# Optimization experiments

Hardware: AMD Instinct MI355X
Metric: run time of the kernel (lower is better)

The kernel has to match this reference:

```python
import jax, jax.numpy as jnp
import numpy as np

DIM, HEADS = 768, 12
HEAD_DIM = DIM // HEADS
SCALE = HEAD_DIM ** -0.5


def setup_inputs() -> dict:
    key = jax.random.key(0)
    ks = jax.random.split(key, 16)
    B, LQ, LK = 8, 512, 512
    s = DIM ** -0.5
    inp = {
        "query": jax.random.normal(ks[0], (B, LQ, DIM), jnp.float32),
        "key_value": jax.random.normal(ks[1], (B, LK, DIM), jnp.float32),
        "query_coords": jax.random.normal(ks[2], (LQ, 2), jnp.float32),
        "key_coords": jax.random.normal(ks[3], (LK, 2), jnp.float32),
        "Wq": jax.random.normal(ks[4], (DIM, DIM), jnp.float32) * s,
        "bq": jnp.zeros((DIM,), jnp.float32),
        "Wk": jax.random.normal(ks[5], (DIM, DIM), jnp.float32) * s,
        "bk": jnp.zeros((DIM,), jnp.float32),
        "Wv": jax.random.normal(ks[6], (DIM, DIM), jnp.float32) * s,
        "bv": jnp.zeros((DIM,), jnp.float32),
        "Wo": jax.random.normal(ks[7], (DIM, DIM), jnp.float32) * s,
        "bo": jnp.zeros((DIM,), jnp.float32),
        "W1": jax.random.normal(ks[8], (6, DIM), jnp.float32) * (6 ** -0.5),
        "b1": jnp.zeros((DIM,), jnp.float32),
        "W2": jax.random.normal(ks[9], (DIM, HEADS), jnp.float32) * s,
        "b2": jnp.zeros((HEADS,), jnp.float32),
    }
    return inp


def reference(query, key_value, query_coords, key_coords,
              Wq, bq, Wk, bk, Wv, bv, Wo, bo, W1, b1, W2, b2):
    B, LQ, _ = query.shape
    LK = key_value.shape[1]
    # QKV projections -> [B, L, H, Dh]
    q = (query @ Wq + bq).reshape(B, LQ, HEADS, HEAD_DIM)
    k = (key_value @ Wk + bk).reshape(B, LK, HEADS, HEAD_DIM)
    v = (key_value @ Wv + bv).reshape(B, LK, HEADS, HEAD_DIM)
    # attention logits [B, H, LQ, LK]
    logits = jnp.einsum('bqhd,bkhd->bhqk', q, k) * SCALE
    # pairwise relative bias: delta [LQ, LK, 2] -> rel [LQ, LK, 6]
    delta = query_coords[:, None, :] - key_coords[None, :, :]
    rel = jnp.concatenate([delta, jnp.abs(delta), jnp.square(delta)], axis=-1)
    hidden = jax.nn.gelu(rel @ W1 + b1, approximate=False)  # [LQ, LK, DIM]
    bias = hidden @ W2 + b2  # [LQ, LK, H]
    logits = logits + jnp.transpose(bias, (2, 0, 1))[None]  # [B,H,LQ,LK]
    weights = jax.nn.softmax(logits, axis=-1)
    out = jnp.einsum('bhqk,bkhd->bqhd', weights, v).reshape(B, LQ, DIM)
    return out @ Wo + bo
```

## Files before the change

kernel.cpp:

```cpp
#include <hip/hip_runtime.h>
#include <hip/hip_bf16.h>
#include <stdint.h>
#include <math.h>

typedef __attribute__((ext_vector_type(4))) float f32x4;
typedef _Float16 f16;
typedef __attribute__((ext_vector_type(8))) _Float16 f16x8;
typedef decltype(__builtin_amdgcn_cvt_pkrtz(0.f, 0.f)) pk16;

#define DIM   768
#define NH    12
#define HD    64
#define NB    8
#define SEQ   512
#define SCALE 0.125f

#define GN    161
#define GPTS  (GN * GN)

#define MFMA16H __builtin_amdgcn_mfma_f32_16x16x32_f16

struct PrepArgs {
    const float* query; const float* key_value; f16* Xq; f16* Xkv;
    const float* W[4]; f16* WT[4];
    const float* W1; const float* b1; const float* W2;
    f16* W1tab; f16* W2tab; float* gtab32;
};

__global__ void __launch_bounds__(256) k_prep(PrepArgs pa) {
    __shared__ float tt[32][33];
    int g = blockIdx.x, t = threadIdx.x;
    if (g < 3072) {
        const float* in = (g < 1536) ? pa.query : pa.key_value;
        f16* out = (g < 1536) ? pa.Xq : pa.Xkv;
        int i = (g % 1536) * 256 + t;
        const float4* s = reinterpret_cast<const float4*>(in + i * 8);
        float4 f0 = s[0], f1 = s[1];
        union { pk16 h[4]; uint4 v; } o;
        o.h[0] = __builtin_amdgcn_cvt_pkrtz(f0.x, f0.y);
        o.h[1] = __builtin_amdgcn_cvt_pkrtz(f0.z, f0.w);
        o.h[2] = __builtin_amdgcn_cvt_pkrtz(f1.x, f1.y);
        o.h[3] = __builtin_amdgcn_cvt_pkrtz(f1.z, f1.w);
        reinterpret_cast<uint4*>(out)[i] = o.v;
    } else if (g < 5376) {
        int bi = g - 3072;
        int z = bi / 576, rem = bi % 576;
        int bx = rem % 24, by = rem / 24;
        const float* W = pa.W[z];
        f16* WT = pa.WT[z];
        int n0 = bx * 32, k0 = by * 32;
        int tx = t & 31, ty = t >> 5;
#pragma unroll
        for (int j = 0; j < 4; ++j)
            tt[ty + 8 * j][tx] = W[(k0 + ty + 8 * j) * DIM + n0 + tx];
        __syncthreads();
#pragma unroll
        for (int j = 0; j < 4; ++j)
            WT[(n0 + ty + 8 * j) * DIM + k0 + tx] = (f16)tt[tx][ty + 8 * j];
    } else {
        int i = (g - 5376) * 256 + t;
        if (i < 3072) {
            int lane = i & 63;
            int hi = lane >> 4, m = lane & 15;
            int u = (i >> 6) * 16 + m;
#pragma unroll
            for (int e = 0; e < 8; ++e) {
                float v = 0.f;
                if (hi == 0) {
                    if (e < 6) v = pa.W1[e * DIM + u];
                    else if (e == 6) v = pa.b1[u];
                }
                pa.W1tab[i * 8 + e] = (f16)v;
            }
        } else if (i < 4608) {
            int i2 = i - 3072;
            int j = i2 >> 6, lane = i2 & 63;
            int gq = lane >> 4, h = lane & 15;
#pragma unroll
            for (int e = 0; e < 8; ++e) {
                int u = 32 * j + ((e >> 2) << 4) + (gq << 2) + (e & 3);
                float v = (h < 12) ? pa.W2[u * 12 + h] : 0.f;
                pa.W2tab[i2 * 8 + e] = (f16)v;
            }
        } else {
            int i2 = i - 4608;
            float x = (i2 + 0.5f) * (1.0f / 256.0f) - 8.0f;
            pa.gtab32[i2] = 0.5f * x * (1.0f + erff(x * 0.70710678f));
        }
    }
}

__global__ void __launch_bounds__(256) k_grid(const f16x8* __restrict__ W1tab,
                                              const f16x8* __restrict__ W2tab,
                                              const float* __restrict__ b2,
                                              const float* __restrict__ gtab32,
                                              f16* __restrict__ grid16) {
    __shared__ float tab[4096];
    int t = threadIdx.x, lane = t & 63, w = t >> 6;
    {
        const uint4* gt = (const uint4*)gtab32;
        uint4* st = (uint4*)tab;
#pragma unroll
        for (int i = 0; i < 4; ++i) st[i * 256 + t] = gt[i * 256 + t];
    }
    int hi = lane >> 4, m = lane & 15;
    int p0 = blockIdx.x * 64 + w * 16;
    int p = p0 + m;
    int gy = p / GN, gx = p - gy * GN;
    float dx = gx * 0.125f - 10.0f;
    float dy = gy * 0.125f - 10.0f;

    union { f16x8 v; pk16 h2[4]; } rf;
    { f16x8 zz = {}; rf.v = zz; }
    if (hi == 0) {
        rf.h2[0] = __builtin_amdgcn_cvt_pkrtz(dx, dy);
        rf.h2[1] = __builtin_amdgcn_cvt_pkrtz(fabsf(dx), fabsf(dy));
        rf.h2[2] = __builtin_amdgcn_cvt_pkrtz(dx * dx, dy * dy);
        rf.h2[3] = __builtin_amdgcn_cvt_pkrtz(1.0f, 0.0f);
    }

    float b2h = (m < 12) ? b2[m] : 0.f;
    f32x4 acc = {b2h, b2h, b2h, b2h};
    const f32x4 zero = {};
    const f16x8* w1p = W1tab + lane;
    const f16x8* w2p = W2tab + lane;
    __syncthreads();

#pragma unroll 2
    for (int j = 0; j < 24; ++j) {
        f16x8 a0  = w1p[(2 * j) * 64];
        f16x8 a1  = w1p[(2 * j + 1) * 64];
        f16x8 w2v = w2p[j * 64];
        f32x4 pre0 = MFMA16H(a0, rf.v, zero, 0, 0, 0);
        f32x4 pre1 = MFMA16H(a1, rf.v, zero, 0, 0, 0);
        float s0[4], s1[4];
#pragma unroll
        for (int e = 0; e < 4; ++e) {
            float x0 = pre0[e];
            float xi0 = __builtin_amdgcn_fmed3f(__builtin_fmaf(x0, 256.f, 2048.f), 0.f, 4095.f);
            float g0 = tab[(int)xi0];
            s0[e] = (x0 > 8.f) ? x0 : g0;
            float x1 = pre1[e];
            float xi1 = __builtin_amdgcn_fmed3f(__builtin_fmaf(x1, 256.f, 2048.f), 0.f, 4095.f);
            float g1 = tab[(int)xi1];
            s1[e] = (x1 > 8.f) ? x1 : g1;
        }
        union { f16x8 v; pk16 h2[4]; } pav;
        pav.h2[0] = __builtin_amdgcn_cvt_pkrtz(s0[0], s0[1]);
        pav.h2[1] = __builtin_amdgcn_cvt_pkrtz(s0[2], s0[3]);
        pav.h2[2] = __builtin_amdgcn_cvt_pkrtz(s1[0], s1[1]);
        pav.h2[3] = __builtin_amdgcn_cvt_pkrtz(s1[2], s1[3]);
        acc = MFMA16H(pav.v, w2v, acc, 0, 0, 0);
    }
    if (m < 12) {
#pragma unroll
        for (int r = 0; r < 4; ++r) {
            int pr = p0 + hi * 4 + r;
            if (pr < GPTS) grid16[pr * 16 + m] = (f16)acc[r];
        }
    }
}

struct MQArgs {
    const float* qc; const float* kc;
    const f16* grid16; f16* bias16;
    const f16* Xq; const f16* Xkv;
    const f16* WqT; const f16* WkT; const f16* WvT;
    const float* bq; const float* bk; const float* bv;
    f16* q_ws; f16* k_ws; f16* v_t;
};

__global__ void __launch_bounds__(256) k_mq3(MQArgs a) {
    __shared__ uint4 lds[1024];
    int bid = blockIdx.x, t = threadIdx.x;
    int lane = t & 63, w = t >> 6;
    int hi = lane >> 4, lm = lane & 15;
    int xcd = bid & 7, slot = bid >> 3;

    if (slot >= 16) {
        int lid = xcd * 288 + (slot - 16);
        int m_group = lid / 36;
        int within = lid - m_group * 36;
        int z = within / 12;
        int n_tile = within - z * 12;
        int m0 = m_group * 64, n0 = n_tile * 64;
        const f16* X = (z == 0) ? a.Xq : a.Xkv;
        const f16* Wt = (z == 0) ? a.WqT : (z == 1) ? a.WkT : a.WvT;
        const float* bias = (z == 0) ? a.bq : (z == 1) ? a.bk : a.bv;
        f16* out = (z == 0) ? a.q_ws : (z == 1) ? a.k_ws : a.v_t;

        int wr = w >> 1, wc = w & 1;
        int srow = t >> 2, sslot = t & 3;
        const f16* Ag = X + (m0 + srow) * DIM + sslot * 8;
        const f16* Bg = Wt + (n0 + srow) * DIM + sslot * 8;
        int wi = srow * 4 + (sslot ^ ((srow >> 1) & 3));

        int aidx[2], bidx[2];
#pragma unroll
        for (int i = 0; i < 2; ++i) {
            int ar = wr * 32 + i * 16 + lm;
            aidx[i] = ar * 4 + (hi ^ ((ar >> 1) & 3));
            int br = wc * 32 + i * 16 + lm;
            bidx[i] = 256 + br * 4 + (hi ^ ((br >> 1) & 3));
        }

        f32x4 acc[2][2] = {};
        lds[wi] = *(const uint4*)(Ag);
        lds[256 + wi] = *(const uint4*)(Bg);
        __syncthreads();

        for (int kt = 0; kt < 24; ++kt) {
            uint4 na, nb;
            bool pf = kt < 23;
            if (pf) {
                na = *(const uint4*)(Ag + (kt + 1) * 32);
                nb = *(const uint4*)(Bg + (kt + 1) * 32);
            }
            int bo = (kt & 1) << 9;
            f16x8 af[2], bf[2];
#pragma unroll
            for (int i = 0; i < 2; ++i) {
                af[i] = *(const f16x8*)&lds[bo + aidx[i]];
                bf[i] = *(const f16x8*)&lds[bo + bidx[i]];
            }
#pragma unroll
            for (int mi = 0; mi < 2; ++mi)
#pragma unroll
                for (int ni = 0; ni < 2; ++ni)
                    acc[mi][ni] = MFMA16H(af[mi], bf[ni], acc[mi][ni], 0, 0, 0);
            if (pf) {
                int bo2 = bo ^ 512;
                lds[bo2 + wi] = na;
                lds[bo2 + 256 + wi] = nb;
                __syncthreads();
            }
        }

#pragma unroll
        for (int mi = 0; mi < 2; ++mi)
#pragma unroll
            for (int ni = 0; ni < 2; ++ni) {
                int n = n0 + wc * 32 + ni * 16 + lm;
                float bn = bias[n];
                int h = n >> 6, d = n & 63;
                int mbase = m0 + wr * 32 + mi * 16 + hi * 4;
                int bb = mbase >> 9, l0 = mbase & 511;
                if (z == 2) {
                    union { pk16 h2[2]; uint2 u2; } o;
                    o.h2[0] = __builtin_amdgcn_cvt_pkrtz(acc[mi][ni][0] + bn, acc[mi][ni][1] + bn);
                    o.h2[1] = __builtin_amdgcn_cvt_pkrtz(acc[mi][ni][2] + bn, acc[mi][ni][3] + bn);
                    *reinterpret_cast<uint2*>(out + (((bb * NH + h) * HD) + d) * SEQ + l0) = o.u2;
                } else {
#pragma unroll
                    for (int r = 0; r < 4; ++r)
                        out[(((bb * NH + h) * SEQ) + l0 + r) * HD + d] = (f16)(acc[mi][ni][r] + bn);
                }
            }
    } else {
        int id = xcd * 16 + slot;
#pragma unroll 2
        for (int i = 0; i < 8; ++i) {
            int p = id * 2048 + i * 256 + t;
            int qi = p >> 9, ki = p & 511;
            float dx = a.qc[2 * qi] - a.kc[2 * ki];
            float dy = a.qc[2 * qi + 1] - a.kc[2 * ki + 1];
            float fxf = __builtin_amdgcn_fmed3f(__builtin_fmaf(dx, 8.f, 80.f), 0.f, 159.9999f);
            float fyf = __builtin_amdgcn_fmed3f(__builtin_fmaf(dy, 8.f, 80.f), 0.f, 159.9999f);
            int ix = (int)fxf, iy = (int)fyf;
            float fx = fxf - (float)ix, fy = fyf - (float)iy;
            const f16* c00 = a.grid16 + (iy * GN + ix) * 16;
            f16x8 g00 = *(const f16x8*)(c00);
            f16x8 g00b = *(const f16x8*)(c00 + 8);
            f16x8 g01 = *(const f16x8*)(c00 + 16);
            f16x8 g01b = *(const f16x8*)(c00 + 24);
            f16x8 g10 = *(const f16x8*)(c00 + GN * 16);
            f16x8 g10b = *(const f16x8*)(c00 + GN * 16 + 8);
            f16x8 g11 = *(const f16x8*)(c00 + GN * 16 + 16);
            f16x8 g11b = *(const f16x8*)(c00 + GN * 16 + 24);
            float o[12];
#pragma unroll
            for (int h = 0; h < 12; ++h) {
                float v00 = (float)(h < 8 ? g00[h] : g00b[h - 8]);
                float v01 = (float)(h < 8 ? g01[h] : g01b[h - 8]);
                float v10 = (float)(h < 8 ? g10[h] : g10b[h - 8]);
                float v11 = (float)(h < 8 ? g11[h] : g11b[h - 8]);
                float v0 = __builtin_fmaf(fx, v01 - v00, v00);
                float v1 = __builtin_fmaf(fx, v11 - v10, v10);
                o[h] = __builtin_fmaf(fy, v1 - v0, v0);
            }
#pragma unroll
            for (int h = 0; h < 12; ++h)
                a.bias16[h * (SEQ * SEQ) + p] = (f16)o[h];
        }
    }
}

__global__ void __launch_bounds__(256) k_gemmO(const f16* __restrict__ X,
                                               const f16* __restrict__ WT,
                                               const float* __restrict__ bias,
                                               float* __restrict__ out) {
    __shared__ uint4 lds[2048];
    int bid = blockIdx.x;
    int xcd = bid & 7, slot = bid >> 3;
    int m0 = (xcd * 4 + slot / 6) * 128, n0 = (slot % 6) * 128;
    int t = threadIdx.x, lane = t & 63, w = t >> 6;
    int wr = w >> 1, wc = w & 1;
    int lm = lane & 15, hi = lane >> 4;

    int srow = t >> 1, sch = t & 1;
    const f16* Ag = X + (m0 + srow) * DIM + sch * 16;
    const f16* Bg = WT + (n0 + srow) * DIM + sch * 16;
    int sw = (srow >> 1) & 3;
    int wiA0 = srow * 4 + ((2 * sch) ^ sw);
    int wiA1 = srow * 4 + ((2 * sch + 1) ^ sw);

    int aidx[4], bidx[4];
#pragma unroll
    for (int i = 0; i < 4; ++i) {
        int ar = wr * 64 + i * 16 + lm;
        aidx[i] = ar * 4 + (hi ^ ((ar >> 1) & 3));
        int br = wc * 64 + i * 16 + lm;
        bidx[i] = 512 + br * 4 + (hi ^ ((br >> 1) & 3));
    }

    f32x4 acc[4][4] = {};
    {
        lds[wiA0] = *(const uint4*)(Ag);
        lds[wiA1] = *(const uint4*)(Ag + 8);
        lds[512 + wiA0] = *(const uint4*)(Bg);
        lds[512 + wiA1] = *(const uint4*)(Bg + 8);
    }
    __syncthreads();

    for (int kt = 0; kt < 24; ++kt) {
        uint4 na0, na1, nb0, nb1;
        bool pf = kt < 23;
        if (pf) {
            const f16* An = Ag + (kt + 1) * 32;
            const f16* Bn = Bg + (kt + 1) * 32;
            na0 = *(const uint4*)(An);
            na1 = *(const uint4*)(An + 8);
            nb0 = *(const uint4*)(Bn);
            nb1 = *(const uint4*)(Bn + 8);
        }
        int bo = (kt & 1) << 10;
        f16x8 af[4], bf[4];
#pragma unroll
        for (int i = 0; i < 4; ++i) {
            af[i] = *(const f16x8*)&lds[bo + aidx[i]];
            bf[i] = *(const f16x8*)&lds[bo + bidx[i]];
        }
#pragma unroll
        for (int mi = 0; mi < 4; ++mi)
#pragma unroll
            for (int ni = 0; ni < 4; ++ni)
                acc[mi][ni] = MFMA16H(af[mi], bf[ni], acc[mi][ni], 0, 0, 0);
        if (pf) {
            int bo2 = bo ^ 1024;
            lds[bo2 + wiA0] = na0; lds[bo2 + wiA1] = na1;
            lds[bo2 + 512 + wiA0] = nb0; lds[bo2 + 512 + wiA1] = nb1;
            __syncthreads();
        }
    }

#pragma unroll
    for (int mi = 0; mi < 4; ++mi)
#pragma unroll
        for (int ni = 0; ni < 4; ++ni) {
            int n = n0 + wc * 64 + ni * 16 + lm;
            float bn = bias[n];
#pragma unroll
            for (int r = 0; r < 4; ++r) {
                int m = m0 + wr * 64 + mi * 16 + hi * 4 + r;
                out[m * DIM + n] = acc[mi][ni][r] + bn;
            }
        }
}

__global__ void __launch_bounds__(256) k_attn4(const f16* __restrict__ q_ws,
                                               const f16* __restrict__ k_ws,
                                               const f16* __restrict__ v_t,
                                               const f16* __restrict__ bias16,
                                               f16* __restrict__ attn_out) {
    __shared__ __align__(16) unsigned short sm16[32 * 520];
    __shared__ float inv32[32];
    int bid = blockIdx.x;
    int xcd = bid & 7, slot = bid >> 3;
    int g = xcd * 12 + (slot >> 4);
    int h = g % 12, b = g / 12;
    int qt = slot & 15;
    int q0 = qt * 32;
    int t = threadIdx.x, lane = t & 63, w = t >> 6;
    int lrow = lane & 15, hi = lane >> 4;
    int bh = b * NH + h;
    const f16* Q = q_ws + (bh * SEQ + q0) * HD;
    const f16* K = k_ws + bh * SEQ * HD;
    const f16* Bias = bias16 + (h * SEQ + q0) * SEQ;

    f16x8 aq[2][2];
#pragma unroll
    for (int rt = 0; rt < 2; ++rt)
#pragma unroll
        for (int ds = 0; ds < 2; ++ds) {
            f16x8 v = *(const f16x8*)(Q + (rt * 16 + lrow) * HD + ds * 32 + hi * 8);
            aq[rt][ds] = v * (f16)SCALE;
        }

#pragma unroll
    for (int ct = 0; ct < 8; ++ct) {
        f32x4 acc0 = {}, acc1 = {};
        int kk = w * 128 + ct * 16 + lrow;
#pragma unroll
        for (int ds = 0; ds < 2; ++ds) {
            f16x8 bk = *(const f16x8*)(K + kk * HD + ds * 32 + hi * 8);
            acc0 = MFMA16H(aq[0][ds], bk, acc0, 0, 0, 0);
            acc1 = MFMA16H(aq[1][ds], bk, acc1, 0, 0, 0);
        }
#pragma unroll
        for (int r = 0; r < 4; ++r) {
            int row0 = hi * 4 + r;
            sm16[row0 * 520 + kk] = (unsigned short)__builtin_bit_cast(unsigned short,
                (f16)(acc0[r] + (float)Bias[row0 * SEQ + kk]));
            int row1 = 16 + hi * 4 + r;
            sm16[row1 * 520 + kk] = (unsigned short)__builtin_bit_cast(unsigned short,
                (f16)(acc1[r] + (float)Bias[row1 * SEQ + kk]));
        }
    }
    __syncthreads();

    {
        int row = t >> 3, seg = t & 7;
        int base = row * 520 + 2 * seg;
        float mx = -1e30f;
#pragma unroll 8
        for (int j = 0; j < 32; ++j) {
            union { uint u; f16 h[2]; } cv;
            cv.u = *(const uint*)&sm16[base + 16 * j];
            mx = fmaxf(mx, fmaxf((float)cv.h[0], (float)cv.h[1]));
        }
        mx = fmaxf(mx, __shfl_xor(mx, 1));
        mx = fmaxf(mx, __shfl_xor(mx, 2));
        mx = fmaxf(mx, __shfl_xor(mx, 4));
        float s = 0.f;
#pragma unroll 8
        for (int j = 0; j < 32; ++j) {
            union { uint u; f16 h[2]; } cv;
            cv.u = *(const uint*)&sm16[base + 16 * j];
            float p0 = __builtin_amdgcn_exp2f(((float)cv.h[0] - mx) * 1.442695041f);
            float p1 = __builtin_amdgcn_exp2f(((float)cv.h[1] - mx) * 1.442695041f);
            s += p0 + p1;
            union { pk16 h; uint u; } o;
            o.h = __builtin_amdgcn_cvt_pkrtz(p0, p1);
            *(uint*)&sm16[base + 16 * j] = o.u;
        }
        s += __shfl_xor(s, 1);
        s += __shfl_xor(s, 2);
        s += __shfl_xor(s, 4);
        if (seg == 0) inv32[row] = 1.0f / s;
    }
    __syncthreads();

    const f16* Vt = v_t + bh * HD * SEQ + (w * 16 + lrow) * SEQ;
    f32x4 oacc0 = {}, oacc1 = {};
    for (int kt = 0; kt < 16; ++kt) {
        f16x8 bv = *(const f16x8*)(Vt + kt * 32 + hi * 8);
        f16x8 pa0 = *(const f16x8*)&sm16[lrow * 520 + kt * 32 + hi * 8];
        f16x8 pa1 = *(const f16x8*)&sm16[(16 + lrow) * 520 + kt * 32 + hi * 8];
        oacc0 = MFMA16H(pa0, bv, oacc0, 0, 0, 0);
        oacc1 = MFMA16H(pa1, bv, oacc1, 0, 0, 0);
    }
#pragma unroll
    for (int r = 0; r < 4; ++r) {
        int row0 = hi * 4 + r;
        float v0 = oacc0[r] * inv32[row0];
        attn_out[(b * SEQ + q0 + row0) * DIM + h * HD + w * 16 + lrow] = (f16)v0;
        int row1 = 16 + hi * 4 + r;
        float v1 = oacc1[r] * inv32[row1];
        attn_out[(b * SEQ + q0 + row1) * DIM + h * HD + w * 16 + lrow] = (f16)v1;
    }
}

extern "C" void kernel_launch(void* const* d_in, const int* in_sizes, int n_in,
                              void* d_out, int out_size, void* d_ws, size_t ws_size,
                              hipStream_t stream) {
    const float* query     = (const float*)d_in[0];
    const float* key_value = (const float*)d_in[1];
    const float* qc        = (const float*)d_in[2];
    const float* kc        = (const float*)d_in[3];
    const float* Wq        = (const float*)d_in[4];
    const float* bq        = (const float*)d_in[5];
    const float* Wk        = (const float*)d_in[6];
    const float* bk        = (const float*)d_in[7];
    const float* Wv        = (const float*)d_in[8];
    const float* bv        = (const float*)d_in[9];
    const float* Wo        = (const float*)d_in[10];
    const float* bo        = (const float*)d_in[11];
    const float* W1        = (const float*)d_in[12];
    const float* b1        = (const float*)d_in[13];
    const float* W2        = (const float*)d_in[14];
    const float* b2        = (const float*)d_in[15];

    char* ws = (char*)d_ws;
    f16* Xq   = (f16*)(ws + 0);
    f16* Xkv  = (f16*)(ws + 6291456);
    f16* WqT  = (f16*)(ws + 12582912);
    f16* WkT  = (f16*)(ws + 13762560);
    f16* WvT  = (f16*)(ws + 14942208);
    f16* WoT  = (f16*)(ws + 16121856);
    f16* q_ws = (f16*)(ws + 17301504);
    f16* k_ws = (f16*)(ws + 23592960);
    f16* v_t  = (f16*)(ws + 29884416);
    f16* bias16   = (f16*)(ws + 36175872);
    f16* W1tab    = (f16*)(ws + 42467328);
    f16* W2tab    = (f16*)(ws + 42516480);
    float* gtab32 = (float*)(ws + 42541056);
    f16* grid16   = (f16*)(ws + 42557440);
    f16* attn_out = Xq;

    PrepArgs pa;
    pa.query = query; pa.key_value = key_value; pa.Xq = Xq; pa.Xkv = Xkv;
    pa.W[0] = Wq; pa.W[1] = Wk; pa.W[2] = Wv; pa.W[3] = Wo;
    pa.WT[0] = WqT; pa.WT[1] = WkT; pa.WT[2] = WvT; pa.WT[3] = WoT;
    pa.W1 = W1; pa.b1 = b1; pa.W2 = W2;
    pa.W1tab = W1tab; pa.W2tab = W2tab; pa.gtab32 = gtab32;
    k_prep<<<dim3(5410), dim3(256), 0, stream>>>(pa);

    k_grid<<<dim3(406), dim3(256), 0, stream>>>((const f16x8*)W1tab, (const f16x8*)W2tab,
                                                b2, gtab32, grid16);

    MQArgs mq;
    mq.qc = qc; mq.kc = kc;
    mq.grid16 = grid16; mq.bias16 = bias16;
    mq.Xq = Xq; mq.Xkv = Xkv;
    mq.WqT = WqT; mq.WkT = WkT; mq.WvT = WvT;
    mq.bq = bq; mq.bk = bk; mq.bv = bv;
    mq.q_ws = q_ws; mq.k_ws = k_ws; mq.v_t = v_t;
    k_mq3<<<dim3(2432), dim3(256), 0, stream>>>(mq);

    k_attn4<<<dim3(1536), dim3(256), 0, stream>>>(q_ws, k_ws, v_t, bias16, attn_out);
    k_gemmO<<<dim3(192), dim3(256), 0, stream>>>(attn_out, WoT, bo, (float*)d_out);
}
```

Baseline: 111.6 us.

## Use direct global-to-LDS loads in QKV GEMM and vectorize attention logit stores

The QKV projection GEMM now stages tiles with global_load_lds, which writes straight into LDS and skips the register round trip. To keep the XOR swizzle, the global source address is permuted instead of the LDS destination. The attention kernel swaps the MFMA operand order so each lane holds four consecutive key columns, which allows vectorized 8-byte bias loads and LDS stores instead of scattered 2-byte accesses. A barrier now runs every iteration, including the last.

Result: slower. 119.6 us (+7.2%).

```diff
diff --git a/kernel.cpp b/kernel.cpp
--- a/kernel.cpp
+++ b/kernel.cpp
@@ -19,6 +19,12 @@
 #define GPTS  (GN * GN)
 
 #define MFMA16H __builtin_amdgcn_mfma_f32_16x16x32_f16
+
+__device__ __forceinline__ void gload_lds16(const void* g, void* l) {
+    __builtin_amdgcn_global_load_lds(
+        (const __attribute__((address_space(1))) uint32_t*)g,
+        (__attribute__((address_space(3))) uint32_t*)l, 16, 0, 0);
+}
 
 struct PrepArgs {
     const float* query; const float* key_value; f16* Xq; f16* Xkv;
@@ -170,7 +176,7 @@
     f16* q_ws; f16* k_ws; f16* v_t;
 };
 
-__global__ void __launch_bounds__(256) k_mq3(MQArgs a) {
+__global__ void __launch_bounds__(256) k_mq6(MQArgs a) {
     __shared__ uint4 lds[1024];
     int bid = blockIdx.x, t = threadIdx.x;
     int lane = t & 63, w = t >> 6;
@@ -190,10 +196,13 @@
         f16* out = (z == 0) ? a.q_ws : (z == 1) ? a.k_ws : a.v_t;
 
         int wr = w >> 1, wc = w & 1;
-        int srow = t >> 2, sslot = t & 3;
-        const f16* Ag = X + (m0 + srow) * DIM + sslot * 8;
-        const f16* Bg = Wt + (n0 + srow) * DIM + sslot * 8;
-        int wi = srow * 4 + (sslot ^ ((srow >> 1) & 3));
+        int chunk = (w << 6) | lane;
+        int srow = chunk >> 2, lslot = chunk & 3;
+        int sslot = lslot ^ ((srow >> 1) & 3);
+        const f16* AgBase = X + (m0 + srow) * DIM + sslot * 8;
+        const f16* BgBase = Wt + (n0 + srow) * DIM + sslot * 8;
+        uint4* ldsA = &lds[w * 64];
+        uint4* ldsB = &lds[256 + w * 64];
 
         int aidx[2], bidx[2];
 #pragma unroll
@@ -205,35 +214,26 @@
         }
 
         f32x4 acc[2][2] = {};
-        lds[wi] = *(const uint4*)(Ag);
-        lds[256 + wi] = *(const uint4*)(Bg);
+        gload_lds16(AgBase, ldsA);
+        gload_lds16(BgBase, ldsB);
         __syncthreads();
 
         for (int kt = 0; kt < 24; ++kt) {
-            uint4 na, nb;
-            bool pf = kt < 23;
-            if (pf) {
-                na = *(const uint4*)(Ag + (kt + 1) * 32);
-                nb = *(const uint4*)(Bg + (kt + 1) * 32);
+            int bo = (kt & 1) << 9;
+            if (kt < 23) {
+                int bo2 = bo ^ 512;
+                gload_lds16(AgBase + (kt + 1) * 32, &lds[bo2] + (ldsA - lds));
+                gload_lds16(BgBase + (kt + 1) * 32, &lds[bo2] + (ldsB - lds));
             }
-            int bo = (kt & 1) << 9;
-            f16x8 af[2], bf[2];
-#pragma unroll
-            for (int i = 0; i < 2; ++i) {
-                af[i] = *(const f16x8*)&lds[bo + aidx[i]];
-                bf[i] = *(const f16x8*)&lds[bo + bidx[i]];
-            }
-#pragma unroll
-            for (int mi = 0; mi < 2; ++mi)
-#pragma unroll
-                for (int ni = 0; ni < 2; ++ni)
-                    acc[mi][ni] = MFMA16H(af[mi], bf[ni], acc[mi][ni], 0, 0, 0);
-            if (pf) {
-                int bo2 = bo ^ 512;
-                lds[bo2 + wi] = na;
-                lds[bo2 + 256 + wi] = nb;
-                __syncthreads();
-            }
+            f16x8 af0 = *(const f16x8*)&lds[bo + aidx[0]];
+            f16x8 af1 = *(const f16x8*)&lds[bo + aidx[1]];
+            f16x8 bf0 = *(const f16x8*)&lds[bo + bidx[0]];
+            f16x8 bf1 = *(const f16x8*)&lds[bo + bidx[1]];
+            acc[0][0] = MFMA16H(af0, bf0, acc[0][0], 0, 0, 0);
+            acc[0][1] = MFMA16H(af0, bf1, acc[0][1], 0, 0, 0);
+            acc[1][0] = MFMA16H(af1, bf0, acc[1][0], 0, 0, 0);
+            acc[1][1] = MFMA16H(af1, bf1, acc[1][1], 0, 0, 0);
+            __syncthreads();
         }
 
 #pragma unroll
@@ -377,7 +377,7 @@
         }
 }
 
-__global__ void __launch_bounds__(256) k_attn4(const f16* __restrict__ q_ws,
+__global__ void __launch_bounds__(256) k_attn5(const f16* __restrict__ q_ws,
                                                const f16* __restrict__ k_ws,
                                                const f16* __restrict__ v_t,
                                                const f16* __restrict__ bias16,
@@ -408,22 +408,25 @@
 
 #pragma unroll
     for (int ct = 0; ct < 8; ++ct) {
-        f32x4 acc0 = {}, acc1 = {};
-        int kk = w * 128 + ct * 16 + lrow;
+        int kbase = w * 128 + ct * 16;
+        f32x4 a0 = {}, a1 = {};
 #pragma unroll
         for (int ds = 0; ds < 2; ++ds) {
-            f16x8 bk = *(const f16x8*)(K + kk * HD + ds * 32 + hi * 8);
-            acc0 = MFMA16H(aq[0][ds], bk, acc0, 0, 0, 0);
-            acc1 = MFMA16H(aq[1][ds], bk, acc1, 0, 0, 0);
-        }
-#pragma unroll
-        for (int r = 0; r < 4; ++r) {
-            int row0 = hi * 4 + r;
-            sm16[row0 * 520 + kk] = (unsigned short)__builtin_bit_cast(unsigned short,
-                (f16)(acc0[r] + (float)Bias[row0 * SEQ + kk]));
-            int row1 = 16 + hi * 4 + r;
-            sm16[row1 * 520 + kk] = (unsigned short)__builtin_bit_cast(unsigned short,
-                (f16)(acc1[r] + (float)Bias[row1 * SEQ + kk]));
+            f16x8 bk = *(const f16x8*)(K + (kbase + lrow) * HD + ds * 32 + hi * 8);
+            a0 = MFMA16H(bk, aq[0][ds], a0, 0, 0, 0);
+            a1 = MFMA16H(bk, aq[1][ds], a1, 0, 0, 0);
+        }
+        int kcol = kbase + hi * 4;
+#pragma unroll
+        for (int rt = 0; rt < 2; ++rt) {
+            f32x4 acc = rt ? a1 : a0;
+            int q = rt * 16 + lrow;
+            union { uint2 u; f16 hh[4]; } bb;
+            bb.u = *(const uint2*)&Bias[q * SEQ + kcol];
+            union { pk16 h2[2]; uint2 u; } o;
+            o.h2[0] = __builtin_amdgcn_cvt_pkrtz(acc[0] + (float)bb.hh[0], acc[1] + (float)bb.hh[1]);
+            o.h2[1] = __builtin_amdgcn_cvt_pkrtz(acc[2] + (float)bb.hh[2], acc[3] + (float)bb.hh[3]);
+            *(uint2*)&sm16[q * 520 + kcol] = o.u;
         }
     }
     __syncthreads();
@@ -434,9 +437,9 @@
         float mx = -1e30f;
 #pragma unroll 8
         for (int j = 0; j < 32; ++j) {
-            union { uint u; f16 h[2]; } cv;
+            union { uint u; f16 hh[2]; } cv;
             cv.u = *(const uint*)&sm16[base + 16 * j];
-            mx = fmaxf(mx, fmaxf((float)cv.h[0], (float)cv.h[1]));
+            mx = fmaxf(mx, fmaxf((float)cv.hh[0], (float)cv.hh[1]));
         }
         mx = fmaxf(mx, __shfl_xor(mx, 1));
         mx = fmaxf(mx, __shfl_xor(mx, 2));
@@ -444,13 +447,13 @@
         float s = 0.f;
 #pragma unroll 8
         for (int j = 0; j < 32; ++j) {
-            union { uint u; f16 h[2]; } cv;
+            union { uint u; f16 hh[2]; } cv;
             cv.u = *(const uint*)&sm16[base + 16 * j];
-            float p0 = __builtin_amdgcn_exp2f(((float)cv.h[0] - mx) * 1.442695041f);
-            float p1 = __builtin_amdgcn_exp2f(((float)cv.h[1] - mx) * 1.442695041f);
+            float p0 = __builtin_amdgcn_exp2f(((float)cv.hh[0] - mx) * 1.442695041f);
+            float p1 = __builtin_amdgcn_exp2f(((float)cv.hh[1] - mx) * 1.442695041f);
             s += p0 + p1;
-            union { pk16 h; uint u; } o;
-            o.h = __builtin_amdgcn_cvt_pkrtz(p0, p1);
+            union { pk16 hh; uint u; } o;
+            o.hh = __builtin_amdgcn_cvt_pkrtz(p0, p1);
             *(uint*)&sm16[base + 16 * j] = o.u;
         }
         s += __shfl_xor(s, 1);
@@ -535,8 +538,8 @@
     mq.WqT = WqT; mq.WkT = WkT; mq.WvT = WvT;
     mq.bq = bq; mq.bk = bk; mq.bv = bv;
     mq.q_ws = q_ws; mq.k_ws = k_ws; mq.v_t = v_t;
-    k_mq3<<<dim3(2432), dim3(256), 0, stream>>>(mq);
-
-    k_attn4<<<dim3(1536), dim3(256), 0, stream>>>(q_ws, k_ws, v_t, bias16, attn_out);
+    k_mq6<<<dim3(2432), dim3(256), 0, stream>>>(mq);
+
+    k_attn5<<<dim3(1536), dim3(256), 0, stream>>>(q_ws, k_ws, v_t, bias16, attn_out);
     k_gemmO<<<dim3(192), dim3(256), 0, stream>>>(attn_out, WoT, bo, (float*)d_out);
 }
```
